# Kernel tuning notes

Measured on AMD Instinct MI355X. Metric: run time of the kernel, lower is better.

Reference implementation:

```python
import jax, jax.numpy as jnp
import numpy as np

# Model dims (Llama-7B-like GQA)
S, B, D_MODEL = 2048, 2, 4096   # total seq, batch, hidden
NH, NKV, HD = 32, 8, 128        # q heads, kv heads, head dim
TP = 4                          # ring size -> number of KV blocks
SB = S // TP                    # KV block length per ring step


def setup_inputs() -> dict:
    key = jax.random.key(0)
    k1, k2, k3 = jax.random.split(key, 3)
    hidden_states = jax.random.normal(k1, (S, B, D_MODEL), jnp.float32)
    w_qkv = jax.random.normal(k2, (D_MODEL, (NH + 2 * NKV) * HD), jnp.float32) / np.sqrt(D_MODEL)
    w_o = jax.random.normal(k3, (NH * HD, D_MODEL), jnp.float32) / np.sqrt(NH * HD)
    return {"hidden_states": hidden_states, "w_qkv": w_qkv, "w_o": w_o}


def _ring_attention(hidden_states, w_qkv, w_o):
    # fused QKV projection: [S,B,D] @ [D,(NH+2*NKV)*HD]
    qkv = hidden_states @ w_qkv
    q, k, v = jnp.split(qkv, [NH * HD, (NH + NKV) * HD], axis=-1)
    q = q.reshape(S, B, NH, HD).transpose(1, 2, 0, 3)    # [B,NH,S,HD]
    k = k.reshape(S, B, NKV, HD).transpose(1, 2, 0, 3)   # [B,NKV,S,HD]
    v = v.reshape(S, B, NKV, HD).transpose(1, 2, 0, 3)

    groups = NH // NKV  # GQA: expand kv heads to match q heads
    k = jnp.repeat(k, groups, axis=1)  # [B,NH,S,HD]
    v = jnp.repeat(v, groups, axis=1)

    scale = 1.0 / np.sqrt(HD)

    # Split K/V along sequence into TP ring blocks: [TP,B,NH,SB,HD]
    k_blocks = k.reshape(B, NH, TP, SB, HD).transpose(2, 0, 1, 3, 4)
    v_blocks = v.reshape(B, NH, TP, SB, HD).transpose(2, 0, 1, 3, 4)

    # Online-softmax (flash-attention style) accumulation over ring steps.
    m0 = jnp.full((B, NH, S), -jnp.inf, q.dtype)   # running row max
    l0 = jnp.zeros((B, NH, S), q.dtype)            # running denom
    acc0 = jnp.zeros((B, NH, S, HD), q.dtype)      # running numerator

    def step(carry, kv):
        m, l, acc = carry
        kb, vb = kv  # [B,NH,SB,HD]
        s = jnp.einsum('bhqd,bhkd->bhqk', q, kb) * scale  # [B,NH,S,SB]
        m_new = jnp.maximum(m, s.max(-1))
        p = jnp.exp(s - m_new[..., None])
        alpha = jnp.exp(m - m_new)
        l = l * alpha + p.sum(-1)
        acc = acc * alpha[..., None] + jnp.einsum('bhqk,bhkd->bhqd', p, vb)
        return (m_new, l, acc), None

    (m, l, acc), _ = jax.lax.scan(step, (m0, l0, acc0), (k_blocks, v_blocks))
    attn = acc / l[..., None]  # [B,NH,S,HD]

    # [B,NH,S,HD] -> [S*B, NH*HD] -> o_proj -> [S,B,D]
    attn = attn.transpose(2, 0, 1, 3).reshape(S * B, NH * HD)
    return (attn @ w_o).reshape(S, B, D_MODEL)


def reference(hidden_states, w_qkv, w_o):
    return _ring_attention(hidden_states, w_qkv, w_o)
```

## Files before the change

kernel.cpp:

```cpp
#include <hip/hip_runtime.h>
#include <hip/hip_bf16.h>


typedef __bf16 bf16x8 __attribute__((ext_vector_type(8)));
typedef float f32x4 __attribute__((ext_vector_type(4)));
typedef unsigned short u16;
typedef u16 u16x4 __attribute__((ext_vector_type(4)));
typedef u16 u16x8 __attribute__((ext_vector_type(8)));
typedef unsigned int u32;

#define SEQ    2048
#define BATCH  2
#define NROWS  4096
#define DM     4096
#define QKVC   6144
#define QSCALE (0.08838834764831845f * 1.4426950408889634f)

__device__ __forceinline__ u16 f2bf(float f) {
  union { float f; u32 u; } v; v.f = f;
  u32 r = v.u + 0x7fffu + ((v.u >> 16) & 1u);
  return (u16)(r >> 16);
}

__device__ __forceinline__ void gload16(const void* g, void* l) {
  __builtin_amdgcn_global_load_lds(
      (const __attribute__((address_space(1))) unsigned int*)g,
      (__attribute__((address_space(3))) unsigned int*)l, 16, 0, 0);
}

__global__ __launch_bounds__(256) void conv_f32_bf16(
    const float* __restrict__ in, u16* __restrict__ out) {
  size_t i = ((size_t)blockIdx.x * 256 + threadIdx.x) * 8;
  float4 a = *(const float4*)(in + i);
  float4 b = *(const float4*)(in + i + 4);
  u16x8 o;
  o[0] = f2bf(a.x); o[1] = f2bf(a.y); o[2] = f2bf(a.z); o[3] = f2bf(a.w);
  o[4] = f2bf(b.x); o[5] = f2bf(b.y); o[6] = f2bf(b.z); o[7] = f2bf(b.w);
  *(u16x8*)(out + i) = o;
}

__global__ __launch_bounds__(256) void transpose_f32_bf16(
    const float* __restrict__ in, u16* __restrict__ out, int K, int N) {
  __shared__ u16 tile[64][65];
  const int k0 = blockIdx.y * 64, n0 = blockIdx.x * 64;
  const int t = threadIdx.x;
#pragma unroll
  for (int i = 0; i < 4; ++i) {
    int slot = i * 256 + t;
    int r = slot >> 4, cq = slot & 15;
    float4 v = *(const float4*)(in + (size_t)(k0 + r) * N + n0 + cq * 4);
    tile[cq * 4 + 0][r] = f2bf(v.x);
    tile[cq * 4 + 1][r] = f2bf(v.y);
    tile[cq * 4 + 2][r] = f2bf(v.z);
    tile[cq * 4 + 3][r] = f2bf(v.w);
  }
  __syncthreads();
#pragma unroll
  for (int i = 0; i < 2; ++i) {
    int slot = i * 256 + t;
    int n = slot >> 3, q = slot & 7;
    u16x8 o;
#pragma unroll
    for (int e = 0; e < 8; ++e) o[e] = tile[n][q * 8 + e];
    *(u16x8*)(out + (size_t)(n0 + n) * K + k0 + q * 8) = o;
  }
}

__global__ __launch_bounds__(256) void vtrans(
    const u16* __restrict__ qkv, u16* __restrict__ vt) {
  __shared__ u16 tile[64][66];
  const int s0 = blockIdx.x * 64, d0 = blockIdx.y * 64;
  const int z = blockIdx.z;
  const int b = z >> 3, kvh = z & 7;
  const int t = threadIdx.x;
#pragma unroll
  for (int i = 0; i < 2; ++i) {
    int chunk = i * 256 + t;
    int r = chunk >> 3, q = chunk & 7;
    u16x8 v = *(const u16x8*)&qkv[(size_t)((s0 + r) * 2 + b) * QKVC + 5120 + kvh * 128 + d0 + q * 8];
#pragma unroll
    for (int e = 0; e < 8; ++e) tile[r][q * 8 + e] = v[e];
  }
  __syncthreads();
#pragma unroll
  for (int i = 0; i < 2; ++i) {
    int chunk = i * 256 + t;
    int d = chunk >> 3, q = chunk & 7;
    u16x8 o;
#pragma unroll
    for (int e = 0; e < 8; ++e) o[e] = tile[q * 8 + e][d];
    *(u16x8*)&vt[(size_t)(z * 128 + d0 + d) * SEQ + s0 + q * 8] = o;
  }
}

template <int CBF16, int SCALEQ>
__global__ __launch_bounds__(512, 2) void gemm192(
    const u16* __restrict__ A, const u16* __restrict__ B,
    void* __restrict__ C, int M, int N, int K, int nby) {
  __shared__ u16 As[3 * 16384];
  __shared__ u16 Bs[2 * 12288];
  const int t = threadIdx.x;
  const int w = t >> 6, l = t & 63;
  const int g = l >> 4, c = l & 15;
  const int wm = w >> 2, wn = w & 3;

  const int nwg = gridDim.x;
  const int sid = (blockIdx.x & 7) * (nwg >> 3) + (blockIdx.x >> 3);
  const int by = sid % nby, bx = sid / nby;
  const int m0 = by * 256, n0 = bx * 192;

  const int gsrc = (l & 7) ^ (l >> 3);
  const u16* pA = A + (size_t)(m0 + w * 8 + (l >> 3)) * K + gsrc * 8;
  const u16* pB = B + (size_t)(n0 + w * 8 + (l >> 3)) * K + gsrc * 8;

#define STG_A192(tt, bb) do {                                               \
    _Pragma("unroll")                                                       \
    for (int u = 0; u < 4; ++u)                                             \
      gload16(pA + (size_t)(u * 64) * K + (size_t)(tt) * 64,                \
              &As[(bb) * 16384 + u * 4096 + w * 512]); } while (0)
#define STG_B192(tt) do { int d_ = (tt) & 1;                                \
    _Pragma("unroll")                                                       \
    for (int u = 0; u < 3; ++u)                                             \
      gload16(pB + (size_t)(u * 64) * K + (size_t)(tt) * 64,                \
              &Bs[d_ * 12288 + u * 4096 + w * 512]); } while (0)

  const int xr0 = ((0 + g) ^ (c & 7)) << 3;
  const int xr1 = ((4 + g) ^ (c & 7)) << 3;

  const f32x4 fz = {0.f, 0.f, 0.f, 0.f};
  f32x4 acc[8][3];
#pragma unroll
  for (int m = 0; m < 8; ++m)
#pragma unroll
    for (int n = 0; n < 3; ++n) acc[m][n] = fz;

  const int nkt = K >> 6;
  STG_A192(0, 0); STG_B192(0);
  STG_A192(1, 1); STG_B192(1);
  asm volatile("s_waitcnt vmcnt(7)" ::: "memory");
  __builtin_amdgcn_sched_barrier(0);
  __builtin_amdgcn_s_barrier();

  int ab = 0;
  for (int tt = 0; tt < nkt; ++tt) {
    const u16* aT = &As[ab * 16384 + (wm * 128 + c) * 64];
    const u16* bT = &Bs[(tt & 1) * 12288 + (wn * 48 + c) * 64];
    bf16x8 a0[4], a1[4], bv[3][2];

#pragma unroll
    for (int m = 0; m < 4; ++m) {
      a0[m] = *(const bf16x8*)(aT + m * 1024 + xr0);
      a1[m] = *(const bf16x8*)(aT + m * 1024 + xr1);
    }
#pragma unroll
    for (int n = 0; n < 3; ++n) {
      bv[n][0] = *(const bf16x8*)(bT + n * 1024 + xr0);
      bv[n][1] = *(const bf16x8*)(bT + n * 1024 + xr1);
    }
    {
      int ab2 = ab + 2; if (ab2 >= 3) ab2 -= 3;
      if (tt + 2 < nkt) STG_A192(tt + 2, ab2);
    }
    __builtin_amdgcn_s_barrier();
    __builtin_amdgcn_s_setprio(1);
#pragma unroll
    for (int m = 0; m < 4; ++m)
#pragma unroll
      for (int n = 0; n < 3; ++n)
        acc[m][n] = __builtin_amdgcn_mfma_f32_16x16x32_bf16(
            a0[m], bv[n][0], acc[m][n], 0, 0, 0);
#pragma unroll
    for (int m = 0; m < 4; ++m)
#pragma unroll
      for (int n = 0; n < 3; ++n)
        acc[m][n] = __builtin_amdgcn_mfma_f32_16x16x32_bf16(
            a1[m], bv[n][1], acc[m][n], 0, 0, 0);
    __builtin_amdgcn_s_setprio(0);
    __builtin_amdgcn_s_barrier();

#pragma unroll
    for (int m = 0; m < 4; ++m) {
      a0[m] = *(const bf16x8*)(aT + (4 + m) * 1024 + xr0);
      a1[m] = *(const bf16x8*)(aT + (4 + m) * 1024 + xr1);
    }
    if (tt + 2 < nkt) {
      STG_B192(tt + 2);
      asm volatile("s_waitcnt vmcnt(7)" ::: "memory");
    } else {
      asm volatile("s_waitcnt vmcnt(0)" ::: "memory");
    }
    __builtin_amdgcn_sched_barrier(0);
    __builtin_amdgcn_s_barrier();
    __builtin_amdgcn_s_setprio(1);
#pragma unroll
    for (int m = 0; m < 4; ++m)
#pragma unroll
      for (int n = 0; n < 3; ++n)
        acc[4 + m][n] = __builtin_amdgcn_mfma_f32_16x16x32_bf16(
            a0[m], bv[n][0], acc[4 + m][n], 0, 0, 0);
#pragma unroll
    for (int m = 0; m < 4; ++m)
#pragma unroll
      for (int n = 0; n < 3; ++n)
        acc[4 + m][n] = __builtin_amdgcn_mfma_f32_16x16x32_bf16(
            a1[m], bv[n][1], acc[4 + m][n], 0, 0, 0);
    __builtin_amdgcn_s_setprio(0);
    __builtin_amdgcn_s_barrier();
    ab = (ab == 2) ? 0 : ab + 1;
  }
#undef STG_A192
#undef STG_B192

#pragma unroll
  for (int m = 0; m < 8; ++m)
#pragma unroll
    for (int n = 0; n < 3; ++n) {
      int row = m0 + wm * 128 + m * 16 + g * 4;
      int col = n0 + wn * 48 + n * 16 + c;
      float sc = (SCALEQ && col < 4096) ? QSCALE : 1.0f;
#pragma unroll
      for (int r = 0; r < 4; ++r) {
        float x = acc[m][n][r] * sc;
        if (CBF16) ((u16*)C)[(size_t)(row + r) * N + col] = f2bf(x);
        else       ((float*)C)[(size_t)(row + r) * N + col] = x;
      }
    }
}

template <int CBF16, int SCALEQ>
__global__ __launch_bounds__(512, 2) void gemm256(
    const u16* __restrict__ A, const u16* __restrict__ B,
    void* __restrict__ C, int M, int N, int K, int nby) {
  __shared__ u16 As[2 * 2 * 8192];
  __shared__ u16 Bs[2 * 2 * 8192];
  const int t = threadIdx.x;
  const int w = t >> 6, l = t & 63;
  const int g = l >> 4, c = l & 15;
  const int wm = w >> 2, wn = w & 3;

  const int nwg = gridDim.x;
  const int sid = (blockIdx.x & 7) * (nwg >> 3) + (blockIdx.x >> 3);
  const int by = sid % nby, bx = sid / nby;
  const int m0 = by * 256, n0 = bx * 256;

  const int gsrc = (l & 7) ^ (l >> 3);
  const u16* pA = A + (size_t)(m0 + w * 8 + (l >> 3)) * K + gsrc * 8;
  const u16* pB = B + (size_t)(n0 + w * 8 + (l >> 3)) * K + gsrc * 8;

#define STG_A(h, tt) do { int d_ = (tt) & 1;                                    \
    gload16(pA + (size_t)((h) * 128) * K + (tt) * 64,                           \
            &As[(d_ * 2 + (h)) * 8192 + w * 512]);                              \
    gload16(pA + (size_t)((h) * 128 + 64) * K + (tt) * 64,                      \
            &As[(d_ * 2 + (h)) * 8192 + 4096 + w * 512]); } while (0)
#define STG_B(h, tt) do { int d_ = (tt) & 1;                                    \
    gload16(pB + (size_t)((h) * 128) * K + (tt) * 64,                           \
            &Bs[(d_ * 2 + (h)) * 8192 + w * 512]);                              \
    gload16(pB + (size_t)((h) * 128 + 64) * K + (tt) * 64,                      \
            &Bs[(d_ * 2 + (h)) * 8192 + 4096 + w * 512]); } while (0)

  const u16* aRd = &As[wm * 8192 + c * 64];
  const u16* bRd = &Bs[(wn >> 1) * 8192 + ((wn & 1) * 64 + c) * 64];
  const int xr0 = ((0 + g) ^ (c & 7)) << 3;
  const int xr1 = ((4 + g) ^ (c & 7)) << 3;

  const f32x4 fz = {0.f, 0.f, 0.f, 0.f};
  f32x4 acc[8][4];
#pragma unroll
  for (int mi = 0; mi < 8; ++mi)
#pragma unroll
    for (int nj = 0; nj < 4; ++nj) acc[mi][nj] = fz;

  const int nkt = K >> 6;
  STG_A(0, 0); STG_A(1, 0); STG_B(0, 0); STG_B(1, 0);
  STG_B(0, 1); STG_B(1, 1);
  asm volatile("s_waitcnt vmcnt(4)" ::: "memory");
  __builtin_amdgcn_sched_barrier(0);
  __builtin_amdgcn_s_barrier();

  for (int tt = 0; tt < nkt; ++tt) {
    const int d = tt & 1;
    const u16* aT = aRd + d * 16384;
    const u16* bT = bRd + d * 16384;
    bf16x8 av[4][2], b01[2][2], b23[2][2];

#pragma unroll
    for (int m = 0; m < 4; ++m) {
      av[m][0] = *(const bf16x8*)(aT + m * 1024 + xr0);
      av[m][1] = *(const bf16x8*)(aT + m * 1024 + xr1);
    }
#pragma unroll
    for (int n = 0; n < 2; ++n) {
      b01[n][0] = *(const bf16x8*)(bT + n * 1024 + xr0);
      b01[n][1] = *(const bf16x8*)(bT + n * 1024 + xr1);
    }
    if (tt + 1 < nkt) STG_A(0, tt + 1);
    __builtin_amdgcn_s_barrier();
    __builtin_amdgcn_s_setprio(1);
#pragma unroll
    for (int kk = 0; kk < 2; ++kk)
#pragma unroll
      for (int m = 0; m < 4; ++m)
#pragma unroll
        for (int n = 0; n < 2; ++n)
          acc[m][n] = __builtin_amdgcn_mfma_f32_16x16x32_bf16(
              av[m][kk], b01[n][kk], acc[m][n], 0, 0, 0);
    __builtin_amdgcn_s_setprio(0);
    __builtin_amdgcn_s_barrier();

#pragma unroll
    for (int n = 0; n < 2; ++n) {
      b23[n][0] = *(const bf16x8*)(bT + (2 + n) * 1024 + xr0);
      b23[n][1] = *(const bf16x8*)(bT + (2 + n) * 1024 + xr1);
    }
    if (tt + 1 < nkt) STG_A(1, tt + 1);
    __builtin_amdgcn_s_barrier();
    __builtin_amdgcn_s_setprio(1);
#pragma unroll
    for (int kk = 0; kk < 2; ++kk)
#pragma unroll
      for (int m = 0; m < 4; ++m)
#pragma unroll
        for (int n = 0; n < 2; ++n)
          acc[m][2 + n] = __builtin_amdgcn_mfma_f32_16x16x32_bf16(
              av[m][kk], b23[n][kk], acc[m][2 + n], 0, 0, 0);
    __builtin_amdgcn_s_setprio(0);
    __builtin_amdgcn_s_barrier();

#pragma unroll
    for (int m = 0; m < 4; ++m) {
      av[m][0] = *(const bf16x8*)(aT + (4 + m) * 1024 + xr0);
      av[m][1] = *(const bf16x8*)(aT + (4 + m) * 1024 + xr1);
    }
    if (tt + 2 < nkt) STG_B(0, tt + 2);
    __builtin_amdgcn_s_barrier();
    __builtin_amdgcn_s_setprio(1);
#pragma unroll
    for (int kk = 0; kk < 2; ++kk)
#pragma unroll
      for (int m = 0; m < 4; ++m)
#pragma unroll
        for (int n = 0; n < 2; ++n)
          acc[4 + m][2 + n] = __builtin_amdgcn_mfma_f32_16x16x32_bf16(
              av[m][kk], b23[n][kk], acc[4 + m][2 + n], 0, 0, 0);
    __builtin_amdgcn_s_setprio(0);
    __builtin_amdgcn_s_barrier();

    if (tt + 2 < nkt) STG_B(1, tt + 2);
    if (tt < nkt - 2) asm volatile("s_waitcnt vmcnt(4)" ::: "memory");
    else              asm volatile("s_waitcnt vmcnt(0)" ::: "memory");
    __builtin_amdgcn_sched_barrier(0);
    __builtin_amdgcn_s_barrier();
    __builtin_amdgcn_s_setprio(1);
#pragma unroll
    for (int kk = 0; kk < 2; ++kk)
#pragma unroll
      for (int m = 0; m < 4; ++m)
#pragma unroll
        for (int n = 0; n < 2; ++n)
          acc[4 + m][n] = __builtin_amdgcn_mfma_f32_16x16x32_bf16(
              av[m][kk], b01[n][kk], acc[4 + m][n], 0, 0, 0);
    __builtin_amdgcn_s_setprio(0);
    __builtin_amdgcn_s_barrier();
  }
#undef STG_A
#undef STG_B

#pragma unroll
  for (int mi = 0; mi < 8; ++mi)
#pragma unroll
    for (int nj = 0; nj < 4; ++nj) {
      int row = m0 + wm * 128 + mi * 16 + g * 4;
      int col = n0 + wn * 64 + nj * 16 + c;
      float sc = (SCALEQ && col < 4096) ? QSCALE : 1.0f;
#pragma unroll
      for (int r = 0; r < 4; ++r) {
        float x = acc[mi][nj][r] * sc;
        if (CBF16) ((u16*)C)[(size_t)(row + r) * N + col] = f2bf(x);
        else       ((float*)C)[(size_t)(row + r) * N + col] = x;
      }
    }
}

__global__ __launch_bounds__(512, 4) void attn_fwd2(
    const u16* __restrict__ qkv, const u16* __restrict__ vtg,
    u16* __restrict__ out) {
  __shared__ u16 Ks[2][64 * 128];
  __shared__ u16 Vs[2][128 * 64];
  __shared__ u16 Ps[8][16 * 64];
  const int t = threadIdx.x;
  const int w = t >> 6, lane = t & 63;
  const int g = lane >> 4, c = lane & 15;
  const int bh = blockIdx.y;
  const int b = bh >> 5, h = bh & 31, kvh = h >> 2;
  const int q0 = blockIdx.x * 128 + w * 16;

  bf16x8 qf[4];
#pragma unroll
  for (int kk = 0; kk < 4; ++kk)
    qf[kk] = *(const bf16x8*)&qkv[(size_t)((q0 + c) * 2 + b) * QKVC + h * 128 + kk * 32 + g * 8];

  const f32x4 fz = {0.f, 0.f, 0.f, 0.f};
  f32x4 acc[8];
#pragma unroll
  for (int db = 0; db < 8; ++db) acc[db] = fz;
  float m_ = -__builtin_inff(), l_ = 0.f;

  const int w4g = w * 4 + g;
  const u16* pK = qkv + (size_t)b * QKVC + 4096 + kvh * 128 + (size_t)((c ^ w4g) & 15) * 8;
  const int vrow = w * 8 + (lane >> 3);
  const u16* pV = vtg + (size_t)(b * 8 + kvh) * 128 * SEQ + (size_t)((lane & 7) ^ (lane >> 3)) * 8;

  auto stage = [&](int bufi, int kv0) {
#pragma unroll
    for (int j = 0; j < 2; ++j)
      gload16(pK + (size_t)(kv0 + j * 32 + w4g) * (2 * QKVC), &Ks[bufi][(j * 8 + w) * 512]);
#pragma unroll
    for (int j = 0; j < 2; ++j)
      gload16(pV + (size_t)(j * 64 + vrow) * SEQ + kv0, &Vs[bufi][(j * 8 + w) * 512]);
  };

  stage(0, 0);
  int buf = 0;
  for (int kv0 = 0; kv0 < SEQ; kv0 += 64) {
    __syncthreads();
    if (kv0 + 64 < SEQ) stage(buf ^ 1, kv0 + 64);

    f32x4 st[4];
    __builtin_amdgcn_s_setprio(1);
#pragma unroll
    for (int kf = 0; kf < 4; ++kf) {
      const u16* kr = &Ks[buf][(kf * 16 + c) * 128];
      bf16x8 kfr[4];
#pragma unroll
      for (int kk = 0; kk < 4; ++kk)
        kfr[kk] = *(const bf16x8*)&kr[(((kk * 4 + g) ^ c) & 15) * 8];
      f32x4 s = fz;
#pragma unroll
      for (int kk = 0; kk < 4; ++kk)
        s = __builtin_amdgcn_mfma_f32_16x16x32_bf16(kfr[kk], qf[kk], s, 0, 0, 0);
      st[kf] = s;
    }
    __builtin_amdgcn_s_setprio(0);

    float mloc = st[0][0];
#pragma unroll
    for (int kf = 0; kf < 4; ++kf)
#pragma unroll
      for (int r = 0; r < 4; ++r) mloc = fmaxf(mloc, st[kf][r]);
    mloc = fmaxf(mloc, __shfl_xor(mloc, 16));
    mloc = fmaxf(mloc, __shfl_xor(mloc, 32));
    if (!__all(mloc - m_ <= 8.0f)) {
      float mnew = fmaxf(m_, mloc);
      float alpha = __builtin_amdgcn_exp2f(m_ - mnew);
      l_ *= alpha;
      f32x4 av;
#pragma unroll
      for (int r = 0; r < 4; ++r) av[r] = __shfl(alpha, g * 4 + r);
#pragma unroll
      for (int db = 0; db < 8; ++db) acc[db] *= av;
      m_ = mnew;
    }
    float ps = 0.f;
#pragma unroll
    for (int kf = 0; kf < 4; ++kf) {
      u16x4 pk;
#pragma unroll
      for (int r = 0; r < 4; ++r) {
        float p = __builtin_amdgcn_exp2f(st[kf][r] - m_);
        ps += p;
        pk[r] = f2bf(p);
      }
      *(u16x4*)&Ps[w][c * 64 + ((((kf * 2 + (g >> 1)) ^ (c & 7)) << 3) | ((g & 1) << 2))] = pk;
    }
    ps += __shfl_xor(ps, 16);
    ps += __shfl_xor(ps, 32);
    l_ += ps;

    bf16x8 pa0 = *(const bf16x8*)&Ps[w][c * 64 + (((0 + g) ^ (c & 7)) << 3)];
    bf16x8 pa1 = *(const bf16x8*)&Ps[w][c * 64 + (((4 + g) ^ (c & 7)) << 3)];
    __builtin_amdgcn_s_setprio(1);
#pragma unroll
    for (int db = 0; db < 8; ++db) {
      const u16* vr = &Vs[buf][(db * 16 + c) * 64];
      bf16x8 v0 = *(const bf16x8*)&vr[(((0 + g) ^ (c & 7)) << 3)];
      bf16x8 v1 = *(const bf16x8*)&vr[(((4 + g) ^ (c & 7)) << 3)];
      acc[db] = __builtin_amdgcn_mfma_f32_16x16x32_bf16(pa0, v0, acc[db], 0, 0, 0);
      acc[db] = __builtin_amdgcn_mfma_f32_16x16x32_bf16(pa1, v1, acc[db], 0, 0, 0);
    }
    __builtin_amdgcn_s_setprio(0);
    buf ^= 1;
  }

  float linv = __builtin_amdgcn_rcpf(l_);
  f32x4 il;
#pragma unroll
  for (int r = 0; r < 4; ++r) il[r] = __shfl(linv, g * 4 + r);
#pragma unroll
  for (int db = 0; db < 8; ++db) {
#pragma unroll
    for (int r = 0; r < 4; ++r) {
      int s = q0 + g * 4 + r;
      out[(size_t)(s * 2 + b) * DM + h * 128 + db * 16 + c] = f2bf(acc[db][r] * il[r]);
    }
  }
}

extern "C" void kernel_launch(void* const* d_in, const int* in_sizes, int n_in,
                              void* d_out, int out_size, void* d_ws, size_t ws_size,
                              hipStream_t stream) {
  const float* hidden = (const float*)d_in[0];
  const float* w_qkv  = (const float*)d_in[1];
  const float* w_o    = (const float*)d_in[2];
  float* outp = (float*)d_out;

  const size_t SZ_X  = (size_t)NROWS * DM * 2;
  const size_t SZ_WQ = (size_t)QKVC * DM * 2;
  const size_t SZ_WO = (size_t)DM * DM * 2;
  const size_t SZ_QKV = (size_t)NROWS * QKVC * 2;
  if (ws_size < SZ_X + SZ_WQ + SZ_WO + SZ_QKV) return;

  char* ws = (char*)d_ws;
  u16* Xb    = (u16*)ws;
  u16* WqkvT = (u16*)(ws + SZ_X);
  u16* WoT   = (u16*)(ws + SZ_X + SZ_WQ);
  u16* QKVb  = (u16*)(ws + SZ_X + SZ_WQ + SZ_WO);
  u16* VtG   = WqkvT;
  u16* Attn  = Xb;

  conv_f32_bf16<<<(NROWS * (size_t)DM) / 2048, 256, 0, stream>>>(hidden, Xb);
  transpose_f32_bf16<<<dim3(QKVC / 64, DM / 64), 256, 0, stream>>>(w_qkv, WqkvT, DM, QKVC);
  transpose_f32_bf16<<<dim3(DM / 64, DM / 64), 256, 0, stream>>>(w_o, WoT, DM, DM);
  gemm192<1, 1><<<512, 512, 0, stream>>>(Xb, WqkvT, QKVb, NROWS, QKVC, DM, 16);
  vtrans<<<dim3(SEQ / 64, 2, 16), 256, 0, stream>>>(QKVb, VtG);
  attn_fwd2<<<dim3(SEQ / 128, BATCH * 32), 512, 0, stream>>>(QKVb, VtG, Attn);
  gemm256<0, 0><<<256, 512, 0, stream>>>(Attn, WoT, outp, NROWS, DM, DM, 16);
}
```

Before: 534.8 us.

## Software-pipeline LDS fragment loads across iterations and triple-buffer A in gemm256

Both GEMM kernels now preload the first A/B register fragments before the loop and load the next iteration's fragments right after the last MFMA block. This lets the MFMAs at the top of each iteration start without waiting on LDS reads. gemm256 gains a third A buffer in shared memory so A tiles can be staged two iterations ahead. The vmcnt waits and barrier placement are retuned to match. The extra LDS (96KB total for gemm256) may limit the two-blocks-per-CU occupancy, and the extra live fragment registers add register pressure.

```diff
diff --git a/kernel.cpp b/kernel.cpp
--- a/kernel.cpp
+++ b/kernel.cpp
@@ -140,73 +140,75 @@
   asm volatile("s_waitcnt vmcnt(7)" ::: "memory");
   __builtin_amdgcn_sched_barrier(0);
   __builtin_amdgcn_s_barrier();
-
-  int ab = 0;
-  for (int tt = 0; tt < nkt; ++tt) {
-    const u16* aT = &As[ab * 16384 + (wm * 128 + c) * 64];
-    const u16* bT = &Bs[(tt & 1) * 12288 + (wn * 48 + c) * 64];
-    bf16x8 a0[4], a1[4], bv[3][2];
-
+  bf16x8 av[4][2], bv[3][2];
+  {
+    const u16* aT = &As[(wm * 128 + c) * 64];
+    const u16* bT = &Bs[(wn * 48 + c) * 64];
 #pragma unroll
     for (int m = 0; m < 4; ++m) {
-      a0[m] = *(const bf16x8*)(aT + m * 1024 + xr0);
-      a1[m] = *(const bf16x8*)(aT + m * 1024 + xr1);
+      av[m][0] = *(const bf16x8*)(aT + m * 1024 + xr0);
+      av[m][1] = *(const bf16x8*)(aT + m * 1024 + xr1);
     }
 #pragma unroll
     for (int n = 0; n < 3; ++n) {
       bv[n][0] = *(const bf16x8*)(bT + n * 1024 + xr0);
       bv[n][1] = *(const bf16x8*)(bT + n * 1024 + xr1);
     }
-    {
-      int ab2 = ab + 2; if (ab2 >= 3) ab2 -= 3;
-      if (tt + 2 < nkt) STG_A192(tt + 2, ab2);
+  }
+
+  int ab = 0;
+  for (int tt = 0; tt < nkt; ++tt) {
+    int ab1 = ab + 1; if (ab1 >= 3) ab1 -= 3;
+    int ab2 = ab + 2; if (ab2 >= 3) ab2 -= 3;
+    const u16* aT = &As[ab * 16384 + (wm * 128 + c) * 64];
+
+    __builtin_amdgcn_s_setprio(1);
+#pragma unroll
+    for (int kk = 0; kk < 2; ++kk)
+#pragma unroll
+      for (int m = 0; m < 4; ++m)
+#pragma unroll
+        for (int n = 0; n < 3; ++n)
+          acc[m][n] = __builtin_amdgcn_mfma_f32_16x16x32_bf16(
+              av[m][kk], bv[n][kk], acc[m][n], 0, 0, 0);
+    __builtin_amdgcn_s_setprio(0);
+    if (tt + 2 < nkt) STG_A192(tt + 2, ab2);
+    if (tt < nkt - 2) asm volatile("s_waitcnt vmcnt(4)" ::: "memory");
+    else              asm volatile("s_waitcnt vmcnt(0)" ::: "memory");
+#pragma unroll
+    for (int m = 0; m < 4; ++m) {
+      av[m][0] = *(const bf16x8*)(aT + (4 + m) * 1024 + xr0);
+      av[m][1] = *(const bf16x8*)(aT + (4 + m) * 1024 + xr1);
     }
     __builtin_amdgcn_s_barrier();
-    __builtin_amdgcn_s_setprio(1);
-#pragma unroll
-    for (int m = 0; m < 4; ++m)
-#pragma unroll
-      for (int n = 0; n < 3; ++n)
-        acc[m][n] = __builtin_amdgcn_mfma_f32_16x16x32_bf16(
-            a0[m], bv[n][0], acc[m][n], 0, 0, 0);
-#pragma unroll
-    for (int m = 0; m < 4; ++m)
-#pragma unroll
-      for (int n = 0; n < 3; ++n)
-        acc[m][n] = __builtin_amdgcn_mfma_f32_16x16x32_bf16(
-            a1[m], bv[n][1], acc[m][n], 0, 0, 0);
-    __builtin_amdgcn_s_setprio(0);
+
+    __builtin_amdgcn_s_setprio(1);
+#pragma unroll
+    for (int kk = 0; kk < 2; ++kk)
+#pragma unroll
+      for (int m = 0; m < 4; ++m)
+#pragma unroll
+        for (int n = 0; n < 3; ++n)
+          acc[4 + m][n] = __builtin_amdgcn_mfma_f32_16x16x32_bf16(
+              av[m][kk], bv[n][kk], acc[4 + m][n], 0, 0, 0);
+    __builtin_amdgcn_s_setprio(0);
+    if (tt + 2 < nkt) STG_B192(tt + 2);
+    if (tt + 1 < nkt) {
+      const u16* aT1 = &As[ab1 * 16384 + (wm * 128 + c) * 64];
+      const u16* bT1 = &Bs[((tt + 1) & 1) * 12288 + (wn * 48 + c) * 64];
+#pragma unroll
+      for (int m = 0; m < 4; ++m) {
+        av[m][0] = *(const bf16x8*)(aT1 + m * 1024 + xr0);
+        av[m][1] = *(const bf16x8*)(aT1 + m * 1024 + xr1);
+      }
+#pragma unroll
+      for (int n = 0; n < 3; ++n) {
+        bv[n][0] = *(const bf16x8*)(bT1 + n * 1024 + xr0);
+        bv[n][1] = *(const bf16x8*)(bT1 + n * 1024 + xr1);
+      }
+    }
     __builtin_amdgcn_s_barrier();
-
-#pragma unroll
-    for (int m = 0; m < 4; ++m) {
-      a0[m] = *(const bf16x8*)(aT + (4 + m) * 1024 + xr0);
-      a1[m] = *(const bf16x8*)(aT + (4 + m) * 1024 + xr1);
-    }
-    if (tt + 2 < nkt) {
-      STG_B192(tt + 2);
-      asm volatile("s_waitcnt vmcnt(7)" ::: "memory");
-    } else {
-      asm volatile("s_waitcnt vmcnt(0)" ::: "memory");
-    }
-    __builtin_amdgcn_sched_barrier(0);
-    __builtin_amdgcn_s_barrier();
-    __builtin_amdgcn_s_setprio(1);
-#pragma unroll
-    for (int m = 0; m < 4; ++m)
-#pragma unroll
-      for (int n = 0; n < 3; ++n)
-        acc[4 + m][n] = __builtin_amdgcn_mfma_f32_16x16x32_bf16(
-            a0[m], bv[n][0], acc[4 + m][n], 0, 0, 0);
-#pragma unroll
-    for (int m = 0; m < 4; ++m)
-#pragma unroll
-      for (int n = 0; n < 3; ++n)
-        acc[4 + m][n] = __builtin_amdgcn_mfma_f32_16x16x32_bf16(
-            a1[m], bv[n][1], acc[4 + m][n], 0, 0, 0);
-    __builtin_amdgcn_s_setprio(0);
-    __builtin_amdgcn_s_barrier();
-    ab = (ab == 2) ? 0 : ab + 1;
+    ab = ab1;
   }
 #undef STG_A192
 #undef STG_B192
@@ -231,7 +233,7 @@
 __global__ __launch_bounds__(512, 2) void gemm256(
     const u16* __restrict__ A, const u16* __restrict__ B,
     void* __restrict__ C, int M, int N, int K, int nby) {
-  __shared__ u16 As[2 * 2 * 8192];
+  __shared__ u16 As[3 * 2 * 8192];
   __shared__ u16 Bs[2 * 2 * 8192];
   const int t = threadIdx.x;
   const int w = t >> 6, l = t & 63;
@@ -247,21 +249,21 @@
   const u16* pA = A + (size_t)(m0 + w * 8 + (l >> 3)) * K + gsrc * 8;
   const u16* pB = B + (size_t)(n0 + w * 8 + (l >> 3)) * K + gsrc * 8;
 
-#define STG_A(h, tt) do { int d_ = (tt) & 1;                                    \
-    gload16(pA + (size_t)((h) * 128) * K + (tt) * 64,                           \
-            &As[(d_ * 2 + (h)) * 8192 + w * 512]);                              \
-    gload16(pA + (size_t)((h) * 128 + 64) * K + (tt) * 64,                      \
-            &As[(d_ * 2 + (h)) * 8192 + 4096 + w * 512]); } while (0)
+#define STG_A(h, tt, bb) do {                                                   \
+    gload16(pA + (size_t)((h) * 128) * K + (size_t)(tt) * 64,                   \
+            &As[((bb) * 2 + (h)) * 8192 + w * 512]);                            \
+    gload16(pA + (size_t)((h) * 128 + 64) * K + (size_t)(tt) * 64,              \
+            &As[((bb) * 2 + (h)) * 8192 + 4096 + w * 512]); } while (0)
 #define STG_B(h, tt) do { int d_ = (tt) & 1;                                    \
-    gload16(pB + (size_t)((h) * 128) * K + (tt) * 64,                           \
+    gload16(pB + (size_t)((h) * 128) * K + (size_t)(tt) * 64,                   \
             &Bs[(d_ * 2 + (h)) * 8192 + w * 512]);                              \
-    gload16(pB + (size_t)((h) * 128 + 64) * K + (tt) * 64,                      \
+    gload16(pB + (size_t)((h) * 128 + 64) * K + (size_t)(tt) * 64,              \
             &Bs[(d_ * 2 + (h)) * 8192 + 4096 + w * 512]); } while (0)
 
-  const u16* aRd = &As[wm * 8192 + c * 64];
-  const u16* bRd = &Bs[(wn >> 1) * 8192 + ((wn & 1) * 64 + c) * 64];
   const int xr0 = ((0 + g) ^ (c & 7)) << 3;
   const int xr1 = ((4 + g) ^ (c & 7)) << 3;
+  const int aoff = wm * 8192 + c * 64;
+  const int boff = (wn >> 1) * 8192 + ((wn & 1) * 64 + c) * 64;
 
   const f32x4 fz = {0.f, 0.f, 0.f, 0.f};
   f32x4 acc[8][4];
@@ -271,18 +273,15 @@
     for (int nj = 0; nj < 4; ++nj) acc[mi][nj] = fz;
 
   const int nkt = K >> 6;
-  STG_A(0, 0); STG_A(1, 0); STG_B(0, 0); STG_B(1, 0);
-  STG_B(0, 1); STG_B(1, 1);
-  asm volatile("s_waitcnt vmcnt(4)" ::: "memory");
+  STG_A(0, 0, 0); STG_A(1, 0, 0); STG_B(0, 0); STG_B(1, 0);
+  STG_A(0, 1, 1); STG_A(1, 1, 1); STG_B(0, 1); STG_B(1, 1);
+  asm volatile("s_waitcnt vmcnt(8)" ::: "memory");
   __builtin_amdgcn_sched_barrier(0);
   __builtin_amdgcn_s_barrier();
-
-  for (int tt = 0; tt < nkt; ++tt) {
-    const int d = tt & 1;
-    const u16* aT = aRd + d * 16384;
-    const u16* bT = bRd + d * 16384;
-    bf16x8 av[4][2], b01[2][2], b23[2][2];
-
+  bf16x8 av[4][2], b01[2][2], b23[2][2];
+  {
+    const u16* aT = &As[aoff];
+    const u16* bT = &Bs[boff];
 #pragma unroll
     for (int m = 0; m < 4; ++m) {
       av[m][0] = *(const bf16x8*)(aT + m * 1024 + xr0);
@@ -293,8 +292,16 @@
       b01[n][0] = *(const bf16x8*)(bT + n * 1024 + xr0);
       b01[n][1] = *(const bf16x8*)(bT + n * 1024 + xr1);
     }
-    if (tt + 1 < nkt) STG_A(0, tt + 1);
-    __builtin_amdgcn_s_barrier();
+  }
+
+  int ab = 0;
+  for (int tt = 0; tt < nkt; ++tt) {
+    int ab1 = ab + 1; if (ab1 >= 3) ab1 -= 3;
+    int ab2 = ab + 2; if (ab2 >= 3) ab2 -= 3;
+    const int bs = tt & 1;
+    const u16* aT = &As[ab * 16384 + aoff];
+    const u16* bT = &Bs[bs * 16384 + boff];
+
     __builtin_amdgcn_s_setprio(1);
 #pragma unroll
     for (int kk = 0; kk < 2; ++kk)
@@ -305,15 +312,14 @@
           acc[m][n] = __builtin_amdgcn_mfma_f32_16x16x32_bf16(
               av[m][kk], b01[n][kk], acc[m][n], 0, 0, 0);
     __builtin_amdgcn_s_setprio(0);
-    __builtin_amdgcn_s_barrier();
-
+    if (tt + 2 < nkt) STG_A(0, tt + 2, ab2);
 #pragma unroll
     for (int n = 0; n < 2; ++n) {
       b23[n][0] = *(const bf16x8*)(bT + (2 + n) * 1024 + xr0);
       b23[n][1] = *(const bf16x8*)(bT + (2 + n) * 1024 + xr1);
     }
-    if (tt + 1 < nkt) STG_A(1, tt + 1);
     __builtin_amdgcn_s_barrier();
+
     __builtin_amdgcn_s_setprio(1);
 #pragma unroll
     for (int kk = 0; kk < 2; ++kk)
@@ -324,15 +330,14 @@
           acc[m][2 + n] = __builtin_amdgcn_mfma_f32_16x16x32_bf16(
               av[m][kk], b23[n][kk], acc[m][2 + n], 0, 0, 0);
     __builtin_amdgcn_s_setprio(0);
-    __builtin_amdgcn_s_barrier();
-
+    if (tt + 2 < nkt) STG_A(1, tt + 2, ab2);
 #pragma unroll
     for (int m = 0; m < 4; ++m) {
       av[m][0] = *(const bf16x8*)(aT + (4 + m) * 1024 + xr0);
       av[m][1] = *(const bf16x8*)(aT + (4 + m) * 1024 + xr1);
     }
-    if (tt + 2 < nkt) STG_B(0, tt + 2);
     __builtin_amdgcn_s_barrier();
+
     __builtin_amdgcn_s_setprio(1);
 #pragma unroll
     for (int kk = 0; kk < 2; ++kk)
@@ -343,13 +348,12 @@
           acc[4 + m][2 + n] = __builtin_amdgcn_mfma_f32_16x16x32_bf16(
               av[m][kk], b23[n][kk], acc[4 + m][2 + n], 0, 0, 0);
     __builtin_amdgcn_s_setprio(0);
-    __builtin_amdgcn_s_barrier();
-
-    if (tt + 2 < nkt) STG_B(1, tt + 2);
-    if (tt < nkt - 2) asm volatile("s_waitcnt vmcnt(4)" ::: "memory");
+    if (tt + 2 < nkt) STG_B(0, tt + 2);
+    if (tt < nkt - 2) asm volatile("s_waitcnt vmcnt(6)" ::: "memory");
     else              asm volatile("s_waitcnt vmcnt(0)" ::: "memory");
     __builtin_amdgcn_sched_barrier(0);
     __builtin_amdgcn_s_barrier();
+
     __builtin_amdgcn_s_setprio(1);
 #pragma unroll
     for (int kk = 0; kk < 2; ++kk)
@@ -360,7 +364,23 @@
           acc[4 + m][n] = __builtin_amdgcn_mfma_f32_16x16x32_bf16(
               av[m][kk], b01[n][kk], acc[4 + m][n], 0, 0, 0);
     __builtin_amdgcn_s_setprio(0);
+    if (tt + 2 < nkt) STG_B(1, tt + 2);
+    if (tt + 1 < nkt) {
+      const u16* aT1 = &As[ab1 * 16384 + aoff];
+      const u16* bT1 = &Bs[(bs ^ 1) * 16384 + boff];
+#pragma unroll
+      for (int m = 0; m < 4; ++m) {
+        av[m][0] = *(const bf16x8*)(aT1 + m * 1024 + xr0);
+        av[m][1] = *(const bf16x8*)(aT1 + m * 1024 + xr1);
+      }
+#pragma unroll
+      for (int n = 0; n < 2; ++n) {
+        b01[n][0] = *(const bf16x8*)(bT1 + n * 1024 + xr0);
+        b01[n][1] = *(const bf16x8*)(bT1 + n * 1024 + xr1);
+      }
+    }
     __builtin_amdgcn_s_barrier();
+    ab = ab1;
   }
 #undef STG_A
 #undef STG_B
```

Result: slower. 625.7 us (+17.0%).
